# Optimization experiments

Measured on AMD Instinct MI355X. Metric: run time of the kernel, lower is better.

Reference implementation:

```python
import jax, jax.numpy as jnp
import numpy as np

D_MODEL, HIDDEN, H, NB = 1024, 128, 16, 32
B, L = 4, 4096


def setup_inputs() -> dict:
    key = jax.random.key(0)
    ks = jax.random.split(key, 6)
    theta_path = jax.random.normal(ks[0], (B, L, H, NB), dtype=jnp.float32)
    content_emb = jax.random.normal(ks[1], (B, L, D_MODEL), dtype=jnp.float32)
    # params (log_Pi init 0.0; final linear weight scaled by 0.01, bias 0, as in torch init)
    log_Pi = jnp.zeros((H, NB), dtype=jnp.float32)
    W1 = jax.random.normal(ks[2], (D_MODEL, HIDDEN), dtype=jnp.float32) / np.sqrt(D_MODEL)
    b1 = jnp.zeros((HIDDEN,), dtype=jnp.float32)
    W2 = (jax.random.normal(ks[3], (HIDDEN, H * NB), dtype=jnp.float32) / np.sqrt(HIDDEN)) * 0.01
    b2 = jnp.zeros((H * NB,), dtype=jnp.float32)
    return {"theta_path": theta_path, "content_emb": content_emb,
            "log_Pi": log_Pi, "W1": W1, "b1": b1, "W2": W2, "b2": b2}


def _affine_combine(c1, c2):
    a1, u1 = c1
    a2, u2 = c2
    return a2 * a1, a2 * u1 + u2


def reference(theta_path, content_emb, log_Pi, W1, b1, W2, b2):
    Bx, Lx, Hx, NBx = theta_path.shape
    # log_R_head: Linear -> GELU(exact) -> Linear, then clamp
    h = jax.nn.gelu(content_emb @ W1 + b1, approximate=False)
    log_R = jnp.clip((h @ W2 + b2).reshape(Bx, Lx, Hx, NBx), -5.0, 5.0)
    R = jnp.exp(log_R)
    # wrapped innovation nu = atan2(sin(-theta), cos(-theta))
    nu = jnp.arctan2(jnp.sin(-theta_path), jnp.cos(-theta_path))
    Pi = jnp.exp(log_Pi)[None, None]            # [1,1,H,NB]
    K = Pi / jnp.maximum(Pi + R, 1e-8)
    alpha = 1.0 - K
    u = K * nu
    # affine recurrence d_t = alpha_t * d_{t-1} + u_t, parallel scan over L
    _, d = jax.lax.associative_scan(_affine_combine, (alpha, u), axis=1)
    return theta_path + d, jnp.broadcast_to(Pi, R.shape), K, R
```

## Files before the change

kernel.cpp:

```cpp
#include <hip/hip_runtime.h>
#include <math.h>

#define B_   4
#define L_   4096
#define C_   512
#define DM_  1024
#define HID_ 128
#define M_   (B_*L_)
#define NC_  256
#define CT_  16

typedef __attribute__((ext_vector_type(8))) short short8;
typedef __attribute__((ext_vector_type(4))) float f32x4;

__device__ __forceinline__ unsigned short f2bf(float f) {
  unsigned u = __float_as_uint(f);
  u += 0x7fffu + ((u >> 16) & 1u);
  return (unsigned short)(u >> 16);
}

__device__ __forceinline__ float wrap_neg(float th) {
  return 6.283185307179586f * rintf(th * 0.15915494309189535f) - th;
}

__global__ __launch_bounds__(256) void k_prep(const float* __restrict__ W1,
                                              const float* __restrict__ W2,
                                              unsigned short* __restrict__ W1T,
                                              unsigned short* __restrict__ W2T) {
  int idx = blockIdx.x * 256 + threadIdx.x;
  if (idx < DM_ * HID_) {
    int n = idx >> 10, k = idx & 1023;
    W1T[idx] = f2bf(W1[(size_t)k * HID_ + n]);
  }
  int i2 = idx - DM_ * HID_;
  if (i2 >= 0 && i2 < HID_ * C_) {
    int n = i2 >> 7, k = i2 & 127;
    W2T[i2] = f2bf(W2[(size_t)k * C_ + n]);
  }
}

__global__ __launch_bounds__(256) void k_mega(const float* __restrict__ X,
                                              const unsigned short* __restrict__ W1T,
                                              const float* __restrict__ b1,
                                              const unsigned short* __restrict__ W2T,
                                              const float* __restrict__ b2,
                                              const float* __restrict__ logPi,
                                              const float* __restrict__ theta,
                                              float* __restrict__ out1,
                                              float* __restrict__ out2,
                                              float* __restrict__ out3,
                                              float* __restrict__ Ab,
                                              float* __restrict__ Ub) {
  __shared__ char lds[8448];
  const int tid  = threadIdx.x;
  const int m0   = blockIdx.x * 16;
  const int lane = tid & 63;
  const int wc   = tid >> 6;
  const int fr   = lane & 15;
  const int kg   = lane >> 4;

  const int srow = tid >> 4;
  const int sk4  = tid & 15;
  const float* xsrc = X + (size_t)(m0 + srow) * DM_ + sk4 * 4;
  f32x4 xr[16];
#pragma unroll
  for (int it = 0; it < 16; ++it)
    xr[it] = __builtin_nontemporal_load((const f32x4*)(xsrc + it * 64));

  const int colbase = wc * 16 + fr;
  const size_t throw0 = (size_t)(m0 + kg * 4) * C_;
  float thr[8][4];
#pragma unroll
  for (int nc = 0; nc < 8; ++nc)
#pragma unroll
    for (int r = 0; r < 4; ++r)
      thr[nc][r] = theta[throw0 + (size_t)r * C_ + nc * 64 + colbase];

  char* swr = lds + srow * 128 + ((sk4 << 3) ^ ((srow & 7) << 4));
  const unsigned short* w1p0 = W1T + (size_t)(wc * 32 + fr) * DM_ + kg * 8;
  const unsigned short* w1p1 = W1T + (size_t)(wc * 32 + 16 + fr) * DM_ + kg * 8;

  f32x4 acc0 = {0.f, 0.f, 0.f, 0.f};
  f32x4 acc1 = {0.f, 0.f, 0.f, 0.f};

  {
    uint2 pk = { f2bf(xr[0][0]) | ((unsigned)f2bf(xr[0][1]) << 16),
                 f2bf(xr[0][2]) | ((unsigned)f2bf(xr[0][3]) << 16) };
    *(uint2*)swr = pk;
  }
  short8 bc[4], bn[4];
  bc[0] = *(const short8*)(w1p0);
  bc[1] = *(const short8*)(w1p1);
  bc[2] = *(const short8*)(w1p0 + 32);
  bc[3] = *(const short8*)(w1p1 + 32);
  __syncthreads();

  const int arow = fr;
  char* ard = lds + arow * 128;

#pragma unroll
  for (int it = 0; it < 16; ++it) {
    const int cur = it & 1;
    if (it < 15) {
      const unsigned short* p0 = w1p0 + (it + 1) * 64;
      const unsigned short* p1 = w1p1 + (it + 1) * 64;
      bn[0] = *(const short8*)(p0);
      bn[1] = *(const short8*)(p1);
      bn[2] = *(const short8*)(p0 + 32);
      bn[3] = *(const short8*)(p1 + 32);
      uint2 pk = { f2bf(xr[it + 1][0]) | ((unsigned)f2bf(xr[it + 1][1]) << 16),
                   f2bf(xr[it + 1][2]) | ((unsigned)f2bf(xr[it + 1][3]) << 16) };
      *(uint2*)(swr + (1 - cur) * 2048) = pk;
    }
#pragma unroll
    for (int ks = 0; ks < 2; ++ks) {
      short8 a = *(const short8*)(ard + cur * 2048 +
                                  (((ks * 4 + kg) << 4) ^ ((arow & 7) << 4)));
      acc0 = __builtin_amdgcn_mfma_f32_16x16x32_bf16(a, bc[ks * 2 + 0], acc0, 0, 0, 0);
      acc1 = __builtin_amdgcn_mfma_f32_16x16x32_bf16(a, bc[ks * 2 + 1], acc1, 0, 0, 0);
    }
    if (it < 15) {
      __syncthreads();
#pragma unroll
      for (int q = 0; q < 4; ++q) bc[q] = bn[q];
    }
  }

#pragma unroll
  for (int j = 0; j < 2; ++j) {
    int col = wc * 32 + j * 16 + fr;
    float bb = b1[col];
    f32x4 av = (j == 0) ? acc0 : acc1;
#pragma unroll
    for (int r = 0; r < 4; ++r) {
      int row = kg * 4 + r;
      float x = av[r] + bb;
      float g = 0.5f * x * (1.0f + erff(x * 0.70710678f));
      *(unsigned short*)(lds + 4096 + row * 272 + col * 2) = f2bf(g);
    }
  }
  __syncthreads();

  const int bidx = blockIdx.x >> 8;
  const int ch   = blockIdx.x & 255;
  const size_t chbase = ((size_t)(bidx * NC_ + ch)) * C_;
  const unsigned short* w2p = W2T + (size_t)colbase * HID_ + kg * 8;
  const char* hrd = lds + 4096 + fr * 272;

  short8 c2[4], n2[4];
#pragma unroll
  for (int ks = 0; ks < 4; ++ks) c2[ks] = *(const short8*)(w2p + ks * 32);

#pragma unroll
  for (int nc = 0; nc < 8; ++nc) {
    const int col = nc * 64 + colbase;
    if (nc < 7) {
#pragma unroll
      for (int ks = 0; ks < 4; ++ks)
        n2[ks] = *(const short8*)(w2p + (size_t)(nc + 1) * 64 * HID_ + ks * 32);
    }
    float Pi = expf(logPi[col]);
    float bb = b2[col];

    f32x4 a2 = {0.f, 0.f, 0.f, 0.f};
#pragma unroll
    for (int ks = 0; ks < 4; ++ks) {
      short8 a = *(const short8*)(hrd + ks * 64 + kg * 16);
      a2 = __builtin_amdgcn_mfma_f32_16x16x32_bf16(a, c2[ks], a2, 0, 0, 0);
    }

    float A = 1.f, U = 0.f;
#pragma unroll
    for (int r = 0; r < 4; ++r) {
      int row = m0 + kg * 4 + r;
      float lr = a2[r] + bb;
      lr = fminf(5.0f, fmaxf(-5.0f, lr));
      float R = expf(lr);
      float K = Pi / fmaxf(Pi + R, 1e-8f);
      size_t o = (size_t)row * C_ + col;
      __builtin_nontemporal_store(Pi, &out1[o]);
      out2[o] = K;
      __builtin_nontemporal_store(R, &out3[o]);
      float nu = wrap_neg(thr[nc][r]);
      float a = 1.f - K;
      U = a * U + K * nu;
      A = a * A;
    }
    float oA = __shfl_xor(A, 16), oU = __shfl_xor(U, 16);
    if ((kg & 1) == 0) { U = oA * U + oU; A = oA * A; }
    else               { U = A * oU + U;  A = A * oA; }
    oA = __shfl_xor(A, 32); oU = __shfl_xor(U, 32);
    if ((kg & 2) == 0) { U = oA * U + oU; A = oA * A; }
    else               { U = A * oU + U;  A = A * oA; }
    if (kg == 0) { Ab[chbase + col] = A; Ub[chbase + col] = U; }

    if (nc < 7) {
#pragma unroll
      for (int ks = 0; ks < 4; ++ks) c2[ks] = n2[ks];
    }
  }
}

__global__ __launch_bounds__(256) void k_scan2(const float* __restrict__ Ab,
                                               const float* __restrict__ Ub,
                                               float* __restrict__ D0) {
  __shared__ float cA[16][17], cU[16][17], carry[16][17];
  const int tid = threadIdx.x;
  const int b   = blockIdx.x >> 5;
  const int c0  = (blockIdx.x & 31) * 16;
  const int c_l = tid & 15, s = tid >> 4;
  const int c   = c0 + c_l;
  float A = 1.f, U = 0.f;
#pragma unroll
  for (int k = 0; k < 16; ++k) {
    size_t o = ((size_t)(b * NC_ + s * 16 + k)) * C_ + c;
    float a = Ab[o], u = Ub[o];
    U = a * U + u; A *= a;
  }
  cA[s][c_l] = A; cU[s][c_l] = U;
  __syncthreads();
  if (tid < 16) {
    float P = 0.f;
#pragma unroll
    for (int ss = 0; ss < 16; ++ss) {
      carry[ss][tid] = P;
      P = cA[ss][tid] * P + cU[ss][tid];
    }
  }
  __syncthreads();
  float d = carry[s][c_l];
#pragma unroll
  for (int k = 0; k < 16; ++k) {
    size_t o = ((size_t)(b * NC_ + s * 16 + k)) * C_ + c;
    D0[o] = d;
    d = Ab[o] * d + Ub[o];
  }
}

__global__ __launch_bounds__(256) void k_scan3(const float* __restrict__ Kv,
                                               const float* __restrict__ theta,
                                               const float* __restrict__ D0,
                                               float* __restrict__ out0) {
  const int g  = blockIdx.x * 256 + threadIdx.x;
  const int cg = g & 127;
  const int ch = (g >> 7) & 255;
  const int b  = g >> 15;
  const int c0 = cg * 4;
  size_t base = ((size_t)b * L_ + (size_t)ch * CT_) * C_ + c0;
  f32x4 d = *(const f32x4*)(D0 + ((size_t)(b * NC_ + ch)) * C_ + c0);
#pragma unroll 4
  for (int j = 0; j < CT_; ++j) {
    size_t idx = base + (size_t)j * C_;
    f32x4 k  = *(const f32x4*)(Kv + idx);
    f32x4 th = *(const f32x4*)(theta + idx);
    f32x4 o;
#pragma unroll
    for (int q = 0; q < 4; ++q) {
      float nu = wrap_neg(th[q]);
      d[q] = (1.f - k[q]) * d[q] + k[q] * nu;
      o[q] = th[q] + d[q];
    }
    __builtin_nontemporal_store(o, (f32x4*)(out0 + idx));
  }
}

extern "C" void kernel_launch(void* const* d_in, const int* in_sizes, int n_in,
                              void* d_out, int out_size, void* d_ws, size_t ws_size,
                              hipStream_t stream) {
  const float* theta = (const float*)d_in[0];
  const float* X     = (const float*)d_in[1];
  const float* logPi = (const float*)d_in[2];
  const float* W1    = (const float*)d_in[3];
  const float* b1    = (const float*)d_in[4];
  const float* W2    = (const float*)d_in[5];
  const float* b2    = (const float*)d_in[6];

  float* out = (float*)d_out;
  const size_t S = (size_t)M_ * C_;
  float* out0 = out;
  float* out1 = out + S;
  float* out2 = out + 2 * S;
  float* out3 = out + 3 * S;

  unsigned short* W1T = (unsigned short*)d_ws;
  unsigned short* W2T = W1T + (size_t)DM_ * HID_;
  float* Ab = (float*)(W2T + (size_t)HID_ * C_);
  float* Ub = Ab + (size_t)B_ * NC_ * C_;
  float* D0 = Ub + (size_t)B_ * NC_ * C_;

  hipLaunchKernelGGL(k_prep, dim3(768), dim3(256), 0, stream, W1, W2, W1T, W2T);
  hipLaunchKernelGGL(k_mega, dim3(M_ / 16), dim3(256), 0, stream,
                     X, W1T, b1, W2T, b2, logPi, theta, out1, out2, out3, Ab, Ub);
  hipLaunchKernelGGL(k_scan2, dim3(B_ * 32), dim3(256), 0, stream, Ab, Ub, D0);
  hipLaunchKernelGGL(k_scan3, dim3(M_ * C_ / 64 / 256), dim3(256), 0, stream,
                     out2, theta, D0, out0);
}
```

Measured before the change: 99.55 us.

## Widen fused GEMM block to 8 waves and move Pi output store to scan3

The fused MLP/gain kernel now runs 512 threads per block. It stages the whole 16x1024 bf16 input tile in LDS once, then each wave computes one 16-column slice of the first GEMM over all of K, with no double-buffered loop and no per-step barriers. In the second GEMM each wave handles 4 column tiles, and theta is loaded per tile instead of held in registers up front. The broadcast Pi output is now written in the final scan kernel rather than in the GEMM kernel, which rebalances store traffic between the two. The trade is more LDS per block (about 37KB), which may limit occupancy, and the W1 fragment prefetching is lost.

```diff
diff --git a/kernel.cpp b/kernel.cpp
--- a/kernel.cpp
+++ b/kernel.cpp
@@ -39,104 +39,70 @@
   }
 }
 
-__global__ __launch_bounds__(256) void k_mega(const float* __restrict__ X,
+__global__ __launch_bounds__(512) void k_mega(const float* __restrict__ X,
                                               const unsigned short* __restrict__ W1T,
                                               const float* __restrict__ b1,
                                               const unsigned short* __restrict__ W2T,
                                               const float* __restrict__ b2,
                                               const float* __restrict__ logPi,
                                               const float* __restrict__ theta,
-                                              float* __restrict__ out1,
                                               float* __restrict__ out2,
                                               float* __restrict__ out3,
                                               float* __restrict__ Ab,
                                               float* __restrict__ Ub) {
-  __shared__ char lds[8448];
+  __shared__ char lds[37120];
   const int tid  = threadIdx.x;
   const int m0   = blockIdx.x * 16;
   const int lane = tid & 63;
-  const int wc   = tid >> 6;
+  const int w    = tid >> 6;
   const int fr   = lane & 15;
   const int kg   = lane >> 4;
 
-  const int srow = tid >> 4;
-  const int sk4  = tid & 15;
-  const float* xsrc = X + (size_t)(m0 + srow) * DM_ + sk4 * 4;
-  f32x4 xr[16];
-#pragma unroll
-  for (int it = 0; it < 16; ++it)
-    xr[it] = __builtin_nontemporal_load((const f32x4*)(xsrc + it * 64));
-
-  const int colbase = wc * 16 + fr;
-  const size_t throw0 = (size_t)(m0 + kg * 4) * C_;
-  float thr[8][4];
-#pragma unroll
-  for (int nc = 0; nc < 8; ++nc)
-#pragma unroll
-    for (int r = 0; r < 4; ++r)
-      thr[nc][r] = theta[throw0 + (size_t)r * C_ + nc * 64 + colbase];
-
-  char* swr = lds + srow * 128 + ((sk4 << 3) ^ ((srow & 7) << 4));
-  const unsigned short* w1p0 = W1T + (size_t)(wc * 32 + fr) * DM_ + kg * 8;
-  const unsigned short* w1p1 = W1T + (size_t)(wc * 32 + 16 + fr) * DM_ + kg * 8;
-
-  f32x4 acc0 = {0.f, 0.f, 0.f, 0.f};
-  f32x4 acc1 = {0.f, 0.f, 0.f, 0.f};
-
   {
-    uint2 pk = { f2bf(xr[0][0]) | ((unsigned)f2bf(xr[0][1]) << 16),
-                 f2bf(xr[0][2]) | ((unsigned)f2bf(xr[0][3]) << 16) };
-    *(uint2*)swr = pk;
-  }
-  short8 bc[4], bn[4];
-  bc[0] = *(const short8*)(w1p0);
-  bc[1] = *(const short8*)(w1p1);
-  bc[2] = *(const short8*)(w1p0 + 32);
-  bc[3] = *(const short8*)(w1p1 + 32);
-  __syncthreads();
-
-  const int arow = fr;
-  char* ard = lds + arow * 128;
-
-#pragma unroll
-  for (int it = 0; it < 16; ++it) {
-    const int cur = it & 1;
-    if (it < 15) {
-      const unsigned short* p0 = w1p0 + (it + 1) * 64;
-      const unsigned short* p1 = w1p1 + (it + 1) * 64;
-      bn[0] = *(const short8*)(p0);
-      bn[1] = *(const short8*)(p1);
-      bn[2] = *(const short8*)(p0 + 32);
-      bn[3] = *(const short8*)(p1 + 32);
-      uint2 pk = { f2bf(xr[it + 1][0]) | ((unsigned)f2bf(xr[it + 1][1]) << 16),
-                   f2bf(xr[it + 1][2]) | ((unsigned)f2bf(xr[it + 1][3]) << 16) };
-      *(uint2*)(swr + (1 - cur) * 2048) = pk;
-    }
-#pragma unroll
-    for (int ks = 0; ks < 2; ++ks) {
-      short8 a = *(const short8*)(ard + cur * 2048 +
-                                  (((ks * 4 + kg) << 4) ^ ((arow & 7) << 4)));
-      acc0 = __builtin_amdgcn_mfma_f32_16x16x32_bf16(a, bc[ks * 2 + 0], acc0, 0, 0, 0);
-      acc1 = __builtin_amdgcn_mfma_f32_16x16x32_bf16(a, bc[ks * 2 + 1], acc1, 0, 0, 0);
-    }
-    if (it < 15) {
-      __syncthreads();
-#pragma unroll
-      for (int q = 0; q < 4; ++q) bc[q] = bn[q];
-    }
-  }
-
-#pragma unroll
-  for (int j = 0; j < 2; ++j) {
-    int col = wc * 32 + j * 16 + fr;
+    const int row = tid >> 5;
+    const int c32 = tid & 31;
+    const float* xsrc = X + (size_t)(m0 + row) * DM_ + c32 * 8;
+    char* base = lds + row * 2048;
+    const int sw = (row & 7) << 4;
+    f32x4 xa[4], xb[4];
+#pragma unroll
+    for (int q = 0; q < 4; ++q) {
+      xa[q] = __builtin_nontemporal_load((const f32x4*)(xsrc + q * 256));
+      xb[q] = __builtin_nontemporal_load((const f32x4*)(xsrc + q * 256 + 4));
+    }
+#pragma unroll
+    for (int q = 0; q < 4; ++q) {
+      uint4 pk;
+      pk.x = f2bf(xa[q][0]) | ((unsigned)f2bf(xa[q][1]) << 16);
+      pk.y = f2bf(xa[q][2]) | ((unsigned)f2bf(xa[q][3]) << 16);
+      pk.z = f2bf(xb[q][0]) | ((unsigned)f2bf(xb[q][1]) << 16);
+      pk.w = f2bf(xb[q][2]) | ((unsigned)f2bf(xb[q][3]) << 16);
+      *(uint4*)(base + ((c32 * 16 + q * 512) ^ sw)) = pk;
+    }
+  }
+  __syncthreads();
+
+  f32x4 acc = {0.f, 0.f, 0.f, 0.f};
+  {
+    const unsigned short* w1p = W1T + (size_t)(w * 16 + fr) * DM_ + kg * 8;
+    const char* ar = lds + fr * 2048;
+    const int asw = (fr & 7) << 4;
+#pragma unroll
+    for (int ks = 0; ks < 32; ++ks) {
+      short8 b = *(const short8*)(w1p + ks * 32);
+      short8 a = *(const short8*)(ar + ((ks * 64 + kg * 16) ^ asw));
+      acc = __builtin_amdgcn_mfma_f32_16x16x32_bf16(a, b, acc, 0, 0, 0);
+    }
+  }
+  {
+    int col = w * 16 + fr;
     float bb = b1[col];
-    f32x4 av = (j == 0) ? acc0 : acc1;
 #pragma unroll
     for (int r = 0; r < 4; ++r) {
       int row = kg * 4 + r;
-      float x = av[r] + bb;
+      float x = acc[r] + bb;
       float g = 0.5f * x * (1.0f + erff(x * 0.70710678f));
-      *(unsigned short*)(lds + 4096 + row * 272 + col * 2) = f2bf(g);
+      *(unsigned short*)(lds + 32768 + row * 272 + col * 2) = f2bf(g);
     }
   }
   __syncthreads();
@@ -144,31 +110,28 @@
   const int bidx = blockIdx.x >> 8;
   const int ch   = blockIdx.x & 255;
   const size_t chbase = ((size_t)(bidx * NC_ + ch)) * C_;
-  const unsigned short* w2p = W2T + (size_t)colbase * HID_ + kg * 8;
-  const char* hrd = lds + 4096 + fr * 272;
-
-  short8 c2[4], n2[4];
-#pragma unroll
-  for (int ks = 0; ks < 4; ++ks) c2[ks] = *(const short8*)(w2p + ks * 32);
-
-#pragma unroll
-  for (int nc = 0; nc < 8; ++nc) {
-    const int col = nc * 64 + colbase;
-    if (nc < 7) {
-#pragma unroll
-      for (int ks = 0; ks < 4; ++ks)
-        n2[ks] = *(const short8*)(w2p + (size_t)(nc + 1) * 64 * HID_ + ks * 32);
-    }
+  const char* hr = lds + 32768 + fr * 272;
+  const size_t throw0 = (size_t)(m0 + kg * 4) * C_;
+
+#pragma unroll
+  for (int t = 0; t < 4; ++t) {
+    const int col = w * 64 + t * 16 + fr;
+    float th[4];
+#pragma unroll
+    for (int r = 0; r < 4; ++r)
+      th[r] = theta[throw0 + (size_t)r * C_ + col];
+
+    const unsigned short* w2p = W2T + (size_t)col * HID_ + kg * 8;
+    f32x4 a2 = {0.f, 0.f, 0.f, 0.f};
+#pragma unroll
+    for (int ks = 0; ks < 4; ++ks) {
+      short8 bfr = *(const short8*)(w2p + ks * 32);
+      short8 afr = *(const short8*)(hr + ks * 64 + kg * 16);
+      a2 = __builtin_amdgcn_mfma_f32_16x16x32_bf16(afr, bfr, a2, 0, 0, 0);
+    }
+
     float Pi = expf(logPi[col]);
     float bb = b2[col];
-
-    f32x4 a2 = {0.f, 0.f, 0.f, 0.f};
-#pragma unroll
-    for (int ks = 0; ks < 4; ++ks) {
-      short8 a = *(const short8*)(hrd + ks * 64 + kg * 16);
-      a2 = __builtin_amdgcn_mfma_f32_16x16x32_bf16(a, c2[ks], a2, 0, 0, 0);
-    }
-
     float A = 1.f, U = 0.f;
 #pragma unroll
     for (int r = 0; r < 4; ++r) {
@@ -178,10 +141,9 @@
       float R = expf(lr);
       float K = Pi / fmaxf(Pi + R, 1e-8f);
       size_t o = (size_t)row * C_ + col;
-      __builtin_nontemporal_store(Pi, &out1[o]);
       out2[o] = K;
       __builtin_nontemporal_store(R, &out3[o]);
-      float nu = wrap_neg(thr[nc][r]);
+      float nu = wrap_neg(th[r]);
       float a = 1.f - K;
       U = a * U + K * nu;
       A = a * A;
@@ -193,11 +155,6 @@
     if ((kg & 2) == 0) { U = oA * U + oU; A = oA * A; }
     else               { U = A * oU + U;  A = A * oA; }
     if (kg == 0) { Ab[chbase + col] = A; Ub[chbase + col] = U; }
-
-    if (nc < 7) {
-#pragma unroll
-      for (int ks = 0; ks < 4; ++ks) c2[ks] = n2[ks];
-    }
   }
 }
 
@@ -240,12 +197,18 @@
 __global__ __launch_bounds__(256) void k_scan3(const float* __restrict__ Kv,
                                                const float* __restrict__ theta,
                                                const float* __restrict__ D0,
-                                               float* __restrict__ out0) {
+                                               const float* __restrict__ logPi,
+                                               float* __restrict__ out0,
+                                               float* __restrict__ out1) {
   const int g  = blockIdx.x * 256 + threadIdx.x;
   const int cg = g & 127;
   const int ch = (g >> 7) & 255;
   const int b  = g >> 15;
   const int c0 = cg * 4;
+  f32x4 lp = *(const f32x4*)(logPi + c0);
+  f32x4 Pi4;
+#pragma unroll
+  for (int q = 0; q < 4; ++q) Pi4[q] = expf(lp[q]);
   size_t base = ((size_t)b * L_ + (size_t)ch * CT_) * C_ + c0;
   f32x4 d = *(const f32x4*)(D0 + ((size_t)(b * NC_ + ch)) * C_ + c0);
 #pragma unroll 4
@@ -261,6 +224,7 @@
       o[q] = th[q] + d[q];
     }
     __builtin_nontemporal_store(o, (f32x4*)(out0 + idx));
+    __builtin_nontemporal_store(Pi4, (f32x4*)(out1 + idx));
   }
 }
 
@@ -289,9 +253,9 @@
   float* D0 = Ub + (size_t)B_ * NC_ * C_;
 
   hipLaunchKernelGGL(k_prep, dim3(768), dim3(256), 0, stream, W1, W2, W1T, W2T);
-  hipLaunchKernelGGL(k_mega, dim3(M_ / 16), dim3(256), 0, stream,
-                     X, W1T, b1, W2T, b2, logPi, theta, out1, out2, out3, Ab, Ub);
+  hipLaunchKernelGGL(k_mega, dim3(M_ / 16), dim3(512), 0, stream,
+                     X, W1T, b1, W2T, b2, logPi, theta, out2, out3, Ab, Ub);
   hipLaunchKernelGGL(k_scan2, dim3(B_ * 32), dim3(256), 0, stream, Ab, Ub, D0);
   hipLaunchKernelGGL(k_scan3, dim3(M_ * C_ / 64 / 256), dim3(256), 0, stream,
-                     out2, theta, D0, out0);
-}
+                     out2, theta, D0, logPi, out0, out1);
+}
```

After: 96.39 us. 3.2% less time.
